# Kernel optimization log

Hardware: AMD Instinct MI355X
Metric: run time of the kernel (lower is better)

Reference implementation:

```python
import jax, jax.numpy as jnp
import numpy as np

COMMITMENT_COST = 0.25
DECAY = 0.99
EPSILON = 1e-05


def setup_inputs() -> dict:
    key = jax.random.key(0)
    k1, k2, k3 = jax.random.split(key, 3)
    B, C, H, W = 64, 64, 64, 64  # C == embedding_dim
    K, D = 1024, 64
    return {
        "inputs": jax.random.normal(k1, (B, C, H, W), dtype=jnp.float32),
        "weight": jax.random.normal(k2, (K, D), dtype=jnp.float32),
        "ema_cluster_size": jnp.ones((K,), dtype=jnp.float32),
        "ema_w": jax.random.normal(k3, (K, D), dtype=jnp.float32),
    }


def reference(inputs, weight, ema_cluster_size, ema_w):
    K, D = weight.shape
    # NCHW -> NHWC, flatten to [N, D]
    x = jnp.transpose(inputs, (0, 2, 3, 1))
    flat = x.reshape(-1, D)
    # squared L2 distances to all codebook entries: [N, K]
    distances = (
        jnp.sum(flat * flat, axis=1, keepdims=True)
        + jnp.sum(weight * weight, axis=1)
        - 2.0 * flat @ weight.T
    )
    idx = jnp.argmin(distances, axis=1)  # [N]
    # training-mode EMA update (replaces the one-hot scatter + matmuls with segment sums)
    counts = jax.ops.segment_sum(jnp.ones_like(idx, dtype=flat.dtype), idx, num_segments=K)
    dw = jax.ops.segment_sum(flat, idx, num_segments=K)  # encodings.T @ flat_input
    cs = ema_cluster_size * DECAY + (1.0 - DECAY) * counts
    n = jnp.sum(cs)
    cs = (cs + EPSILON) / (n + K * EPSILON) * n  # Laplace smoothing
    ew = ema_w * DECAY + (1.0 - DECAY) * dw
    new_weight = ew / cs[:, None]
    # quantize with the UPDATED codebook (matches in-place torch order)
    quantized = new_weight[idx].reshape(x.shape)
    e_latent_loss = jnp.mean(jnp.square(jax.lax.stop_gradient(quantized) - x))
    loss = COMMITMENT_COST * e_latent_loss
    quantized_st = x + jax.lax.stop_gradient(quantized - x)  # straight-through
    return loss, jnp.transpose(quantized_st, (0, 3, 1, 2)), idx[:, None]
```

## Files before the change

### kernel.cpp

```cpp
#include <hip/hip_runtime.h>

#define K_CODES 1024
#define D_DIM   64
#define N_ROWS  262144
#define HW      4096
#define CHW     262144
#define N_ELEM  16777216
#define DECAY   0.99f
#define OMD     0.01f
#define EPS_F   1e-05f
#define MARGIN_ACC 0.001f
#define FLAG_CAP 32768
#define SEG_CAP  2048
#define NHB      64
#define BROWS    128

typedef __attribute__((ext_vector_type(8))) short bf16x8;
typedef __attribute__((ext_vector_type(4))) float f32x4;

constexpr size_t OFF_LOSS    = 0;
constexpr size_t OFF_FLAGCNT = 8;
constexpr size_t OFF_DONE    = 12;
constexpr size_t OFF_W2F     = 64;
constexpr size_t OFF_W2D     = 4160;
constexpr size_t OFF_CS      = 12352;
constexpr size_t OFF_GOFF    = 16448;
constexpr size_t OFF_NEWW    = 282752;
constexpr size_t OFF_IDX     = 544896;
constexpr size_t OFF_HISTB   = 1593472;
constexpr size_t OFF_SORT    = 1855616;
constexpr size_t OFF_FLAGS   = 1855616;
constexpr size_t OFF_WFRAG   = 1986688;

__device__ __forceinline__ short f2bf(float f) {
    unsigned u = __float_as_uint(f);
    u += 0x7fffu + ((u >> 16) & 1u);
    return (short)(u >> 16);
}
__device__ __forceinline__ float bf2f(short h) {
    return __uint_as_float(((unsigned)(unsigned short)h) << 16);
}

__device__ __forceinline__ void gload_lds16(const float4* g, void* l) {
    __builtin_amdgcn_global_load_lds(
        (const __attribute__((address_space(1))) void*)g,
        (__attribute__((address_space(3))) void*)l, 16, 0, 0);
}

__global__ __launch_bounds__(256) void prep_kernel(
    const float* __restrict__ w, short* __restrict__ wfrag,
    float* __restrict__ w2f, double* __restrict__ w2d,
    int* __restrict__ zero16) {
    int t = threadIdx.x;
    if (blockIdx.x == 35 && t < 4) zero16[t] = 0;
    if (blockIdx.x < 32) {
        int gid = blockIdx.x * 256 + t;
        int j = gid >> 7, h = (gid >> 6) & 1, L = gid & 63;
        int code = j * 16 + (L & 15);
        int kb = h * 32 + ((L >> 4) << 3);
        const float* wp = w + code * D_DIM + kb;
        short hi[8], lo[8];
#pragma unroll
        for (int i = 0; i < 8; ++i) {
            float v = wp[i];
            short hb = f2bf(v);
            hi[i] = hb;
            lo[i] = f2bf(v - bf2f(hb));
        }
        short* dh = wfrag + (size_t)(((j * 2 + h) * 2 + 0) * 64 + L) * 8;
        short* dl = wfrag + (size_t)(((j * 2 + h) * 2 + 1) * 64 + L) * 8;
#pragma unroll
        for (int i = 0; i < 8; ++i) { dh[i] = hi[i]; dl[i] = lo[i]; }
    } else {
        int k = (blockIdx.x - 32) * 256 + t;
        const float* wk = w + k * D_DIM;
        float sf = 0.f; double sd = 0.0;
#pragma unroll
        for (int d = 0; d < D_DIM; ++d) {
            float wv = wk[d];
            sf = fmaf(wv, wv, sf);
            sd = fma((double)wv, (double)wv, sd);
        }
        w2f[k] = sf; w2d[k] = sd;
    }
}

__global__ __launch_bounds__(256) __attribute__((amdgpu_waves_per_eu(2, 4)))
void argmin_kernel(
    const float* __restrict__ inp, const short* __restrict__ wfrag,
    const float* __restrict__ w2f, int* __restrict__ idx_ws,
    float* __restrict__ out_idx_f, float* __restrict__ xt,
    int* __restrict__ flagcnt, int* __restrict__ flaglist) {
    __shared__ float w2s[K_CODES];
    __shared__ alignas(16) char smem_u[64 * 68 * 4];
    __shared__ alignas(16) short bufA[8192];
    float (*xs)[68] = (float (*)[68])smem_u;
    short* bufB = (short*)smem_u;

    int t = threadIdx.x;
    ((float4*)w2s)[t] = ((const float4*)w2f)[t];

    int rowbase = blockIdx.x * BROWS;
    int b = rowbase >> 12, hwb = rowbase & (HW - 1);
    const float* xp = inp + (size_t)b * CHW + hwb;
    int lane = t & 63, wave = t >> 6;
    int q = lane >> 4, col = lane & 15;

    bf16x8 aH[2][2], aL[2][2];

    for (int p = 0; p < 2; ++p) {
#pragma unroll
        for (int it = 0; it < 16; ++it) {
            int d = wave * 16 + it;
            xs[lane][d] = xp[(size_t)d * HW + p * 64 + lane];
        }
        __syncthreads();

        float4* xt4 = (float4*)(xt + (size_t)(rowbase + p * 64) * D_DIM);
#pragma unroll
        for (int i2 = 0; i2 < 4; ++i2) {
            int c2 = t + i2 * 256;
            xt4[c2] = ((const float4*)xs[c2 >> 4])[c2 & 15];
        }

        if ((wave >> 1) == p) {
#pragma unroll
            for (int s2 = 0; s2 < 2; ++s2) {
                int rl = (wave & 1) * 32 + s2 * 16 + col;
#pragma unroll
                for (int h = 0; h < 2; ++h) {
#pragma unroll
                    for (int i = 0; i < 8; ++i) {
                        float v = xs[rl][h * 32 + q * 8 + i];
                        short hb = f2bf(v);
                        aH[s2][h][i] = hb;
                        aL[s2][h][i] = f2bf(v - bf2f(hb));
                    }
                }
            }
        }
        __syncthreads();
    }

    float best[2][4], best2[2][4];
    int   bj[2][4];
#pragma unroll
    for (int s2 = 0; s2 < 2; ++s2)
#pragma unroll
        for (int r = 0; r < 4; ++r) {
            best[s2][r] = -3.4e38f; best2[s2][r] = -3.4e38f; bj[s2][r] = 0;
        }
    const float4* wsrc = (const float4*)wfrag;

    {
        const float4* src = wsrc + t;
        char* nb = (char*)bufA + wave * 1024;
#pragma unroll
        for (int i2 = 0; i2 < 4; ++i2)
            gload_lds16(src + i2 * 256, nb + i2 * 4096);
    }

    for (int st = 0; st < 16; ++st) {
        asm volatile("s_waitcnt vmcnt(0)" ::: "memory");
        __syncthreads();
        if (st < 15) {
            const float4* src = wsrc + (size_t)(st + 1) * 1024 + t;
            char* nb = ((st & 1) ? (char*)bufA : (char*)bufB) + wave * 1024;
#pragma unroll
            for (int i2 = 0; i2 < 4; ++i2)
                gload_lds16(src + i2 * 256, nb + i2 * 4096);
        }
        const bf16x8* wt = (const bf16x8*)((st & 1) ? bufB : bufA);

#pragma unroll
        for (int jp = 0; jp < 2; ++jp) {
            int jA = st * 4 + jp * 2, jB = jA + 1;
            int jjA = jp * 2, jjB = jp * 2 + 1;
            bf16x8 bh0A = wt[(jjA * 4 + 0) * 64 + lane];
            bf16x8 bl0A = wt[(jjA * 4 + 1) * 64 + lane];
            bf16x8 bh1A = wt[(jjA * 4 + 2) * 64 + lane];
            bf16x8 bl1A = wt[(jjA * 4 + 3) * 64 + lane];
            bf16x8 bh0B = wt[(jjB * 4 + 0) * 64 + lane];
            bf16x8 bl0B = wt[(jjB * 4 + 1) * 64 + lane];
            bf16x8 bh1B = wt[(jjB * 4 + 2) * 64 + lane];
            bf16x8 bl1B = wt[(jjB * 4 + 3) * 64 + lane];
            float cA = -0.5f * w2s[jA * 16 + col];
            float cB = -0.5f * w2s[jB * 16 + col];
            f32x4 a0A = {cA, cA, cA, cA}, a1A = {cA, cA, cA, cA};
            f32x4 a0B = {cB, cB, cB, cB}, a1B = {cB, cB, cB, cB};
            a0A = __builtin_amdgcn_mfma_f32_16x16x32_bf16(aL[0][0], bh0A, a0A, 0, 0, 0);
            a1A = __builtin_amdgcn_mfma_f32_16x16x32_bf16(aL[1][0], bh0A, a1A, 0, 0, 0);
            a0B = __builtin_amdgcn_mfma_f32_16x16x32_bf16(aL[0][0], bh0B, a0B, 0, 0, 0);
            a1B = __builtin_amdgcn_mfma_f32_16x16x32_bf16(aL[1][0], bh0B, a1B, 0, 0, 0);
            a0A = __builtin_amdgcn_mfma_f32_16x16x32_bf16(aL[0][1], bh1A, a0A, 0, 0, 0);
            a1A = __builtin_amdgcn_mfma_f32_16x16x32_bf16(aL[1][1], bh1A, a1A, 0, 0, 0);
            a0B = __builtin_amdgcn_mfma_f32_16x16x32_bf16(aL[0][1], bh1B, a0B, 0, 0, 0);
            a1B = __builtin_amdgcn_mfma_f32_16x16x32_bf16(aL[1][1], bh1B, a1B, 0, 0, 0);
            a0A = __builtin_amdgcn_mfma_f32_16x16x32_bf16(aH[0][0], bl0A, a0A, 0, 0, 0);
            a1A = __builtin_amdgcn_mfma_f32_16x16x32_bf16(aH[1][0], bl0A, a1A, 0, 0, 0);
            a0B = __builtin_amdgcn_mfma_f32_16x16x32_bf16(aH[0][0], bl0B, a0B, 0, 0, 0);
            a1B = __builtin_amdgcn_mfma_f32_16x16x32_bf16(aH[1][0], bl0B, a1B, 0, 0, 0);
            a0A = __builtin_amdgcn_mfma_f32_16x16x32_bf16(aH[0][1], bl1A, a0A, 0, 0, 0);
            a1A = __builtin_amdgcn_mfma_f32_16x16x32_bf16(aH[1][1], bl1A, a1A, 0, 0, 0);
            a0B = __builtin_amdgcn_mfma_f32_16x16x32_bf16(aH[0][1], bl1B, a0B, 0, 0, 0);
            a1B = __builtin_amdgcn_mfma_f32_16x16x32_bf16(aH[1][1], bl1B, a1B, 0, 0, 0);
            a0A = __builtin_amdgcn_mfma_f32_16x16x32_bf16(aH[0][0], bh0A, a0A, 0, 0, 0);
            a1A = __builtin_amdgcn_mfma_f32_16x16x32_bf16(aH[1][0], bh0A, a1A, 0, 0, 0);
            a0B = __builtin_amdgcn_mfma_f32_16x16x32_bf16(aH[0][0], bh0B, a0B, 0, 0, 0);
            a1B = __builtin_amdgcn_mfma_f32_16x16x32_bf16(aH[1][0], bh0B, a1B, 0, 0, 0);
            a0A = __builtin_amdgcn_mfma_f32_16x16x32_bf16(aH[0][1], bh1A, a0A, 0, 0, 0);
            a1A = __builtin_amdgcn_mfma_f32_16x16x32_bf16(aH[1][1], bh1A, a1A, 0, 0, 0);
            a0B = __builtin_amdgcn_mfma_f32_16x16x32_bf16(aH[0][1], bh1B, a0B, 0, 0, 0);
            a1B = __builtin_amdgcn_mfma_f32_16x16x32_bf16(aH[1][1], bh1B, a1B, 0, 0, 0);
#pragma unroll
            for (int s2 = 0; s2 < 2; ++s2) {
#pragma unroll
                for (int r = 0; r < 4; ++r) {
                    float vA = (s2 ? a1A : a0A)[r];
                    float vB = (s2 ? a1B : a0B)[r];
                    bool gA = vA > best[s2][r];
                    best2[s2][r] = fmaxf(best2[s2][r], fminf(best[s2][r], vA));
                    best[s2][r]  = fmaxf(best[s2][r], vA);
                    bj[s2][r]    = gA ? jA : bj[s2][r];
                    bool gB = vB > best[s2][r];
                    best2[s2][r] = fmaxf(best2[s2][r], fminf(best[s2][r], vB));
                    best[s2][r]  = fmaxf(best[s2][r], vB);
                    bj[s2][r]    = gB ? jB : bj[s2][r];
                }
            }
        }
    }

    int bk[2][4];
#pragma unroll
    for (int s2 = 0; s2 < 2; ++s2)
#pragma unroll
        for (int r = 0; r < 4; ++r)
            bk[s2][r] = (bj[s2][r] << 4) | col;

#pragma unroll
    for (int m = 1; m < 16; m <<= 1) {
#pragma unroll
        for (int s2 = 0; s2 < 2; ++s2) {
#pragma unroll
            for (int r = 0; r < 4; ++r) {
                float ob  = __shfl_xor(best[s2][r], m, 64);
                float ob2 = __shfl_xor(best2[s2][r], m, 64);
                int   obk = __shfl_xor(bk[s2][r], m, 64);
                float nb2 = fmaxf(fmaxf(best2[s2][r], ob2),
                                  fminf(best[s2][r], ob));
                int   nbk = ob > best[s2][r] ? obk
                            : (best[s2][r] > ob ? bk[s2][r]
                                                : min(bk[s2][r], obk));
                best[s2][r]  = fmaxf(best[s2][r], ob);
                best2[s2][r] = nb2;
                bk[s2][r]    = nbk;
            }
        }
    }

    if (col == 0) {
#pragma unroll
        for (int s2 = 0; s2 < 2; ++s2) {
#pragma unroll
            for (int r = 0; r < 4; ++r) {
                int row = rowbase + wave * 32 + s2 * 16 + q * 4 + r;
                idx_ws[row]    = bk[s2][r];
                out_idx_f[row] = (float)bk[s2][r];
                if (best[s2][r] - best2[s2][r] < MARGIN_ACC) {
                    int pos = atomicAdd(flagcnt, 1);
                    if (pos < FLAG_CAP) flaglist[pos] = row;
                }
            }
        }
    }
}

__global__ __launch_bounds__(256) void refine_kernel(
    const float* __restrict__ xt, const float* __restrict__ weight,
    const double* __restrict__ w2d, int* __restrict__ idx_ws,
    float* __restrict__ out_idx_f, const int* __restrict__ flagcnt,
    const int* __restrict__ flaglist) {
    __shared__ float sx[4][64];
    int cnt = *flagcnt;
    if (cnt > FLAG_CAP) cnt = FLAG_CAP;
    int t = threadIdx.x, lane = t & 63, wave = t >> 6;

    for (int r = blockIdx.x * 4 + wave; r < cnt; r += gridDim.x * 4) {
        int row = flaglist[r];
        sx[wave][lane] = xt[(size_t)row * D_DIM + lane];
        asm volatile("s_waitcnt lgkmcnt(0)" ::: "memory");

        double bd = 1.0e300; int bi = 0;
        int k0 = lane * 16;
#pragma unroll 4
        for (int c = 0; c < 16; ++c) {
            int k = k0 + c;
            const float4* wk4 = (const float4*)(weight + (size_t)k * D_DIM);
            double dot = 0.0;
#pragma unroll
            for (int d4 = 0; d4 < 16; ++d4) {
                float4 wv = wk4[d4];
                dot = fma((double)wv.x, (double)sx[wave][d4 * 4 + 0], dot);
                dot = fma((double)wv.y, (double)sx[wave][d4 * 4 + 1], dot);
                dot = fma((double)wv.z, (double)sx[wave][d4 * 4 + 2], dot);
                dot = fma((double)wv.w, (double)sx[wave][d4 * 4 + 3], dot);
            }
            double dist = w2d[k] - 2.0 * dot;
            if (dist < bd) { bd = dist; bi = k; }
        }
#pragma unroll
        for (int m = 1; m < 64; m <<= 1) {
            double od = __shfl_xor(bd, m, 64);
            int    oi = __shfl_xor(bi, m, 64);
            if (od < bd || (od == bd && oi < bi)) { bd = od; bi = oi; }
        }
        if (lane == 0 && bi != idx_ws[row]) {
            idx_ws[row]    = bi;
            out_idx_f[row] = (float)bi;
        }
    }
}

__global__ __launch_bounds__(1024) void hist_kernel(
    const int* __restrict__ idx_ws, int* __restrict__ histb) {
    __shared__ int h[K_CODES];
    int t = threadIdx.x, b = blockIdx.x;
    h[t] = 0;
    __syncthreads();
    int4 c = ((const int4*)idx_ws)[b * 1024 + t];
    atomicAdd(&h[c.x], 1); atomicAdd(&h[c.y], 1);
    atomicAdd(&h[c.z], 1); atomicAdd(&h[c.w], 1);
    __syncthreads();
    histb[b * K_CODES + t] = h[t];
}

__global__ __launch_bounds__(1024) void scan_kernel(
    int* __restrict__ histb, int* __restrict__ goff,
    const float* __restrict__ ema_cs, float* __restrict__ csbuf) {
    __shared__ int pre[K_CODES];
    __shared__ float red[K_CODES];
    int k = threadIdx.x;

    int s = 0;
    for (int b = 0; b < NHB; ++b) {
        int v = histb[b * K_CODES + k];
        histb[b * K_CODES + k] = s;
        s += v;
    }
    int cnt = s;

    pre[k] = cnt;
    __syncthreads();
    for (int d = 1; d < K_CODES; d <<= 1) {
        int v = (k >= d) ? pre[k - d] : 0;
        __syncthreads();
        if (k >= d) pre[k] += v;
        __syncthreads();
    }
    int base = pre[k] - cnt;
    goff[k] = base;
    if (k == K_CODES - 1) goff[K_CODES] = pre[k];

    for (int b = 0; b < NHB; ++b) histb[b * K_CODES + k] += base;

    float cs = ema_cs[k] * DECAY + OMD * (float)cnt;
    red[k] = cs;
    __syncthreads();
    for (int s2 = 512; s2 > 0; s2 >>= 1) {
        if (k < s2) red[k] += red[k + s2];
        __syncthreads();
    }
    float n = red[0];
    csbuf[k] = (cs + EPS_F) / (n + (float)K_CODES * EPS_F) * n;
}

__global__ __launch_bounds__(1024) void scatter_kernel(
    const int* __restrict__ idx_ws, const int* __restrict__ histb,
    int* __restrict__ sorted) {
    __shared__ int cur[K_CODES];
    int t = threadIdx.x, b = blockIdx.x;
    cur[t] = histb[b * K_CODES + t];
    __syncthreads();
    int4 c = ((const int4*)idx_ws)[b * 1024 + t];
    int r0 = (b * 1024 + t) * 4;
    sorted[atomicAdd(&cur[c.x], 1)] = r0 + 0;
    sorted[atomicAdd(&cur[c.y], 1)] = r0 + 1;
    sorted[atomicAdd(&cur[c.z], 1)] = r0 + 2;
    sorted[atomicAdd(&cur[c.w], 1)] = r0 + 3;
}

__global__ __launch_bounds__(512) void dwred_kernel(
    const float* __restrict__ xt, const int* __restrict__ sorted,
    const int* __restrict__ goff, const float* __restrict__ ema_w,
    const float* __restrict__ csbuf, float* __restrict__ new_w) {
    __shared__ int   rows[SEG_CAP];
    __shared__ float red[512];
    int k = blockIdx.x, t = threadIdx.x;
    int base = goff[k];
    int cnt = goff[k + 1] - base;
    int cc = cnt > SEG_CAP ? SEG_CAP : cnt;

    for (int i = t; i < cc; i += 512) rows[i] = sorted[base + i];
    __syncthreads();

    int d = t & 63, sub = t >> 6;
    float a0 = 0.f, a1 = 0.f;
    int i = sub;
    for (; i + 8 < cc; i += 16) {
        a0 += xt[(size_t)rows[i] * D_DIM + d];
        a1 += xt[(size_t)rows[i + 8] * D_DIM + d];
    }
    for (; i < cc; i += 8) a0 += xt[(size_t)rows[i] * D_DIM + d];
    red[t] = a0 + a1;
    __syncthreads();
    if (t < 64) {
        float dwv = red[t] + red[t + 64] + red[t + 128] + red[t + 192] +
                    red[t + 256] + red[t + 320] + red[t + 384] + red[t + 448];
        new_w[k * D_DIM + t] =
            (ema_w[k * D_DIM + t] * DECAY + OMD * dwv) / csbuf[k];
    }
}

__global__ __launch_bounds__(256) void out_kernel(
    const float* __restrict__ inp, const float* __restrict__ new_w,
    const int* __restrict__ idx_ws, float* __restrict__ out,
    double* __restrict__ loss_acc, int* __restrict__ done_cnt) {
    int row = blockIdx.x * 256 + threadIdx.x;
    int b  = row >> 12;
    int hw = row & (HW - 1);
    const float* xp = inp + (size_t)b * CHW + hw;
    float* op = out + 1 + (size_t)b * CHW + hw;

    int k = idx_ws[row];
    const float4* qp4 = (const float4*)(new_w + (size_t)k * D_DIM);

    float lsum = 0.f;
#pragma unroll
    for (int d4 = 0; d4 < 16; ++d4) {
        float4 qq = qp4[d4];
#pragma unroll
        for (int j = 0; j < 4; ++j) {
            int d = d4 * 4 + j;
            float xv = xp[(size_t)d * HW];
            float qv = (j == 0) ? qq.x : (j == 1) ? qq.y : (j == 2) ? qq.z : qq.w;
            float diff = qv - xv;
            lsum = fmaf(diff, diff, lsum);
            op[(size_t)d * HW] = xv + diff;
        }
    }

    __shared__ double lred[256];
    lred[threadIdx.x] = (double)lsum;
    __syncthreads();
    for (int s = 128; s > 0; s >>= 1) {
        if (threadIdx.x < s) lred[threadIdx.x] += lred[threadIdx.x + s];
        __syncthreads();
    }
    if (threadIdx.x == 0) {
        atomicAdd(loss_acc, lred[0]);
        __threadfence();
        int old = atomicAdd(done_cnt, 1);
        if (old == (int)gridDim.x - 1) {
            double v = atomicAdd(loss_acc, 0.0);
            out[0] = (float)(0.25 * (v / (double)N_ELEM));
        }
    }
}

extern "C" void kernel_launch(void* const* d_in, const int* in_sizes, int n_in,
                              void* d_out, int out_size, void* d_ws, size_t ws_size,
                              hipStream_t stream) {
    const float* inp    = (const float*)d_in[0];
    const float* weight = (const float*)d_in[1];
    const float* ema_cs = (const float*)d_in[2];
    const float* ema_w  = (const float*)d_in[3];
    float* out = (float*)d_out;

    char* ws = (char*)d_ws;
    double* loss_acc = (double*)(ws + OFF_LOSS);
    int*    flagcnt  = (int*)(ws + OFF_FLAGCNT);
    int*    done_cnt = (int*)(ws + OFF_DONE);
    float*  w2f      = (float*)(ws + OFF_W2F);
    double* w2d      = (double*)(ws + OFF_W2D);
    float*  csbuf    = (float*)(ws + OFF_CS);
    int*    goff     = (int*)(ws + OFF_GOFF);
    float*  new_w    = (float*)(ws + OFF_NEWW);
    int*    idx_ws   = (int*)(ws + OFF_IDX);
    int*    histb    = (int*)(ws + OFF_HISTB);
    int*    sorted   = (int*)(ws + OFF_SORT);
    int*    flaglist = (int*)(ws + OFF_FLAGS);
    short*  wfrag    = (short*)(ws + OFF_WFRAG);

    float* xt        = out + 1;
    float* out_idx_f = out + 1 + (size_t)N_ELEM;

    prep_kernel<<<36, 256, 0, stream>>>(weight, wfrag, w2f, w2d, (int*)ws);

    argmin_kernel<<<N_ROWS / BROWS, 256, 0, stream>>>(
        inp, wfrag, w2f, idx_ws, out_idx_f, xt, flagcnt, flaglist);

    refine_kernel<<<1024, 256, 0, stream>>>(
        xt, weight, w2d, idx_ws, out_idx_f, flagcnt, flaglist);

    hist_kernel<<<NHB, 1024, 0, stream>>>(idx_ws, histb);

    scan_kernel<<<1, 1024, 0, stream>>>(histb, goff, ema_cs, csbuf);

    scatter_kernel<<<NHB, 1024, 0, stream>>>(idx_ws, histb, sorted);

    dwred_kernel<<<K_CODES, 512, 0, stream>>>(xt, sorted, goff, ema_w, csbuf, new_w);

    out_kernel<<<N_ROWS / 256, 256, 0, stream>>>(inp, new_w, idx_ws, out,
                                                 loss_acc, done_cnt);
}
```

Measured before the change: 387.3 us.

## Fuse code histogram into argmin/refine via global atomics, drop hist kernel

Per-code counts are now accumulated with global atomicAdd directly in the argmin kernel, and the refine kernel corrects them when it changes an index. This removes the separate histogram kernel and the 64-block per-block prefix pass. The scatter becomes a one-row-per-thread global-atomic cursor scatter instead of a per-block LDS cursor scatter. The refine dot product is also split into two accumulators to shorten the fp64 FMA dependency chain. The cost is heavy global atomic contention on 1024 counters: 262144 increments during argmin and again during scatter.

```diff
diff --git a/kernel.cpp b/kernel.cpp
--- a/kernel.cpp
+++ b/kernel.cpp
@@ -12,7 +12,6 @@
 #define MARGIN_ACC 0.001f
 #define FLAG_CAP 32768
 #define SEG_CAP  2048
-#define NHB      64
 #define BROWS    128
 
 typedef __attribute__((ext_vector_type(8))) short bf16x8;
@@ -25,9 +24,10 @@
 constexpr size_t OFF_W2D     = 4160;
 constexpr size_t OFF_CS      = 12352;
 constexpr size_t OFF_GOFF    = 16448;
+constexpr size_t OFF_CNT     = 20608;
 constexpr size_t OFF_NEWW    = 282752;
 constexpr size_t OFF_IDX     = 544896;
-constexpr size_t OFF_HISTB   = 1593472;
+constexpr size_t OFF_GCUR    = 1593472;
 constexpr size_t OFF_SORT    = 1855616;
 constexpr size_t OFF_FLAGS   = 1855616;
 constexpr size_t OFF_WFRAG   = 1986688;
@@ -50,9 +50,12 @@
 __global__ __launch_bounds__(256) void prep_kernel(
     const float* __restrict__ w, short* __restrict__ wfrag,
     float* __restrict__ w2f, double* __restrict__ w2d,
-    int* __restrict__ zero16) {
+    int* __restrict__ scalars, int* __restrict__ cnt) {
     int t = threadIdx.x;
-    if (blockIdx.x == 35 && t < 4) zero16[t] = 0;
+    if (blockIdx.x == 35) {
+        if (t < 4) scalars[t] = 0;
+        cnt[t] = 0; cnt[t + 256] = 0; cnt[t + 512] = 0; cnt[t + 768] = 0;
+    }
     if (blockIdx.x < 32) {
         int gid = blockIdx.x * 256 + t;
         int j = gid >> 7, h = (gid >> 6) & 1, L = gid & 63;
@@ -90,7 +93,8 @@
     const float* __restrict__ inp, const short* __restrict__ wfrag,
     const float* __restrict__ w2f, int* __restrict__ idx_ws,
     float* __restrict__ out_idx_f, float* __restrict__ xt,
-    int* __restrict__ flagcnt, int* __restrict__ flaglist) {
+    int* __restrict__ flagcnt, int* __restrict__ flaglist,
+    int* __restrict__ cnt) {
     __shared__ float w2s[K_CODES];
     __shared__ alignas(16) char smem_u[64 * 68 * 4];
     __shared__ alignas(16) short bufA[8192];
@@ -265,8 +269,10 @@
 #pragma unroll
             for (int r = 0; r < 4; ++r) {
                 int row = rowbase + wave * 32 + s2 * 16 + q * 4 + r;
-                idx_ws[row]    = bk[s2][r];
-                out_idx_f[row] = (float)bk[s2][r];
+                int k = bk[s2][r];
+                idx_ws[row]    = k;
+                out_idx_f[row] = (float)k;
+                atomicAdd(&cnt[k], 1);
                 if (best[s2][r] - best2[s2][r] < MARGIN_ACC) {
                     int pos = atomicAdd(flagcnt, 1);
                     if (pos < FLAG_CAP) flaglist[pos] = row;
@@ -280,33 +286,38 @@
     const float* __restrict__ xt, const float* __restrict__ weight,
     const double* __restrict__ w2d, int* __restrict__ idx_ws,
     float* __restrict__ out_idx_f, const int* __restrict__ flagcnt,
-    const int* __restrict__ flaglist) {
+    const int* __restrict__ flaglist, int* __restrict__ cnt) {
     __shared__ float sx[4][64];
-    int cnt = *flagcnt;
-    if (cnt > FLAG_CAP) cnt = FLAG_CAP;
+    int fc = *flagcnt;
+    if (fc > FLAG_CAP) fc = FLAG_CAP;
     int t = threadIdx.x, lane = t & 63, wave = t >> 6;
 
-    for (int r = blockIdx.x * 4 + wave; r < cnt; r += gridDim.x * 4) {
+    for (int r = blockIdx.x * 4 + wave; r < fc; r += gridDim.x * 4) {
         int row = flaglist[r];
         sx[wave][lane] = xt[(size_t)row * D_DIM + lane];
         asm volatile("s_waitcnt lgkmcnt(0)" ::: "memory");
 
         double bd = 1.0e300; int bi = 0;
         int k0 = lane * 16;
-#pragma unroll 4
+#pragma unroll 2
         for (int c = 0; c < 16; ++c) {
             int k = k0 + c;
             const float4* wk4 = (const float4*)(weight + (size_t)k * D_DIM);
-            double dot = 0.0;
-#pragma unroll
-            for (int d4 = 0; d4 < 16; ++d4) {
-                float4 wv = wk4[d4];
-                dot = fma((double)wv.x, (double)sx[wave][d4 * 4 + 0], dot);
-                dot = fma((double)wv.y, (double)sx[wave][d4 * 4 + 1], dot);
-                dot = fma((double)wv.z, (double)sx[wave][d4 * 4 + 2], dot);
-                dot = fma((double)wv.w, (double)sx[wave][d4 * 4 + 3], dot);
+            double dotA = 0.0, dotB = 0.0;
+#pragma unroll
+            for (int d4 = 0; d4 < 8; ++d4) {
+                float4 wa = wk4[d4];
+                float4 wb = wk4[d4 + 8];
+                dotA = fma((double)wa.x, (double)sx[wave][d4 * 4 + 0], dotA);
+                dotB = fma((double)wb.x, (double)sx[wave][d4 * 4 + 32], dotB);
+                dotA = fma((double)wa.y, (double)sx[wave][d4 * 4 + 1], dotA);
+                dotB = fma((double)wb.y, (double)sx[wave][d4 * 4 + 33], dotB);
+                dotA = fma((double)wa.z, (double)sx[wave][d4 * 4 + 2], dotA);
+                dotB = fma((double)wb.z, (double)sx[wave][d4 * 4 + 34], dotB);
+                dotA = fma((double)wa.w, (double)sx[wave][d4 * 4 + 3], dotA);
+                dotB = fma((double)wb.w, (double)sx[wave][d4 * 4 + 35], dotB);
             }
-            double dist = w2d[k] - 2.0 * dot;
+            double dist = w2d[k] - 2.0 * (dotA + dotB);
             if (dist < bd) { bd = dist; bi = k; }
         }
 #pragma unroll
@@ -315,42 +326,27 @@
             int    oi = __shfl_xor(bi, m, 64);
             if (od < bd || (od == bd && oi < bi)) { bd = od; bi = oi; }
         }
-        if (lane == 0 && bi != idx_ws[row]) {
-            idx_ws[row]    = bi;
-            out_idx_f[row] = (float)bi;
-        }
-    }
-}
-
-__global__ __launch_bounds__(1024) void hist_kernel(
-    const int* __restrict__ idx_ws, int* __restrict__ histb) {
-    __shared__ int h[K_CODES];
-    int t = threadIdx.x, b = blockIdx.x;
-    h[t] = 0;
-    __syncthreads();
-    int4 c = ((const int4*)idx_ws)[b * 1024 + t];
-    atomicAdd(&h[c.x], 1); atomicAdd(&h[c.y], 1);
-    atomicAdd(&h[c.z], 1); atomicAdd(&h[c.w], 1);
-    __syncthreads();
-    histb[b * K_CODES + t] = h[t];
+        if (lane == 0) {
+            int old = idx_ws[row];
+            if (bi != old) {
+                idx_ws[row]    = bi;
+                out_idx_f[row] = (float)bi;
+                atomicSub(&cnt[old], 1);
+                atomicAdd(&cnt[bi], 1);
+            }
+        }
+    }
 }
 
 __global__ __launch_bounds__(1024) void scan_kernel(
-    int* __restrict__ histb, int* __restrict__ goff,
-    const float* __restrict__ ema_cs, float* __restrict__ csbuf) {
+    const int* __restrict__ cnt, int* __restrict__ goff,
+    int* __restrict__ gcur, const float* __restrict__ ema_cs,
+    float* __restrict__ csbuf) {
     __shared__ int pre[K_CODES];
     __shared__ float red[K_CODES];
     int k = threadIdx.x;
-
-    int s = 0;
-    for (int b = 0; b < NHB; ++b) {
-        int v = histb[b * K_CODES + k];
-        histb[b * K_CODES + k] = s;
-        s += v;
-    }
-    int cnt = s;
-
-    pre[k] = cnt;
+    int c = cnt[k];
+    pre[k] = c;
     __syncthreads();
     for (int d = 1; d < K_CODES; d <<= 1) {
         int v = (k >= d) ? pre[k - d] : 0;
@@ -358,17 +354,16 @@
         if (k >= d) pre[k] += v;
         __syncthreads();
     }
-    int base = pre[k] - cnt;
+    int base = pre[k] - c;
     goff[k] = base;
+    gcur[k] = base;
     if (k == K_CODES - 1) goff[K_CODES] = pre[k];
 
-    for (int b = 0; b < NHB; ++b) histb[b * K_CODES + k] += base;
-
-    float cs = ema_cs[k] * DECAY + OMD * (float)cnt;
+    float cs = ema_cs[k] * DECAY + OMD * (float)c;
     red[k] = cs;
     __syncthreads();
-    for (int s2 = 512; s2 > 0; s2 >>= 1) {
-        if (k < s2) red[k] += red[k + s2];
+    for (int s = 512; s > 0; s >>= 1) {
+        if (k < s) red[k] += red[k + s];
         __syncthreads();
     }
     float n = red[0];
@@ -376,18 +371,11 @@
 }
 
 __global__ __launch_bounds__(1024) void scatter_kernel(
-    const int* __restrict__ idx_ws, const int* __restrict__ histb,
+    const int* __restrict__ idx_ws, int* __restrict__ gcur,
     int* __restrict__ sorted) {
-    __shared__ int cur[K_CODES];
-    int t = threadIdx.x, b = blockIdx.x;
-    cur[t] = histb[b * K_CODES + t];
-    __syncthreads();
-    int4 c = ((const int4*)idx_ws)[b * 1024 + t];
-    int r0 = (b * 1024 + t) * 4;
-    sorted[atomicAdd(&cur[c.x], 1)] = r0 + 0;
-    sorted[atomicAdd(&cur[c.y], 1)] = r0 + 1;
-    sorted[atomicAdd(&cur[c.z], 1)] = r0 + 2;
-    sorted[atomicAdd(&cur[c.w], 1)] = r0 + 3;
+    int r = blockIdx.x * 1024 + threadIdx.x;
+    int k = idx_ws[r];
+    sorted[atomicAdd(&gcur[k], 1)] = r;
 }
 
 __global__ __launch_bounds__(512) void dwred_kernel(
@@ -485,9 +473,10 @@
     double* w2d      = (double*)(ws + OFF_W2D);
     float*  csbuf    = (float*)(ws + OFF_CS);
     int*    goff     = (int*)(ws + OFF_GOFF);
+    int*    cnt      = (int*)(ws + OFF_CNT);
     float*  new_w    = (float*)(ws + OFF_NEWW);
     int*    idx_ws   = (int*)(ws + OFF_IDX);
-    int*    histb    = (int*)(ws + OFF_HISTB);
+    int*    gcur     = (int*)(ws + OFF_GCUR);
     int*    sorted   = (int*)(ws + OFF_SORT);
     int*    flaglist = (int*)(ws + OFF_FLAGS);
     short*  wfrag    = (short*)(ws + OFF_WFRAG);
@@ -495,19 +484,17 @@
     float* xt        = out + 1;
     float* out_idx_f = out + 1 + (size_t)N_ELEM;
 
-    prep_kernel<<<36, 256, 0, stream>>>(weight, wfrag, w2f, w2d, (int*)ws);
+    prep_kernel<<<36, 256, 0, stream>>>(weight, wfrag, w2f, w2d, (int*)ws, cnt);
 
     argmin_kernel<<<N_ROWS / BROWS, 256, 0, stream>>>(
-        inp, wfrag, w2f, idx_ws, out_idx_f, xt, flagcnt, flaglist);
+        inp, wfrag, w2f, idx_ws, out_idx_f, xt, flagcnt, flaglist, cnt);
 
     refine_kernel<<<1024, 256, 0, stream>>>(
-        xt, weight, w2d, idx_ws, out_idx_f, flagcnt, flaglist);
-
-    hist_kernel<<<NHB, 1024, 0, stream>>>(idx_ws, histb);
-
-    scan_kernel<<<1, 1024, 0, stream>>>(histb, goff, ema_cs, csbuf);
-
-    scatter_kernel<<<NHB, 1024, 0, stream>>>(idx_ws, histb, sorted);
+        xt, weight, w2d, idx_ws, out_idx_f, flagcnt, flaglist, cnt);
+
+    scan_kernel<<<1, 1024, 0, stream>>>(cnt, goff, gcur, ema_cs, csbuf);
+
+    scatter_kernel<<<N_ROWS / 1024, 1024, 0, stream>>>(idx_ws, gcur, sorted);
 
     dwred_kernel<<<K_CODES, 512, 0, stream>>>(xt, sorted, goff, ema_w, csbuf, new_w);
 
```

Result: slower. 529.5 us (+36.7%).
